# Kernel optimization log

Measured on AMD Instinct MI355X. Metric: run time of the kernel, lower is better.

The kernel has to match this reference:

```python
import jax, jax.numpy as jnp
import numpy as np

EPS = 1e-7
ROUTING_ITERS = 3

def squash(s, axis=-1):
    # v = (|s|^2 / (1+|s|^2)) * s / |s|
    sq = jnp.sum(jnp.square(s), axis=axis, keepdims=True)
    return (sq / (1.0 + sq)) * s / jnp.sqrt(sq + EPS)

def setup_inputs() -> dict:
    key = jax.random.key(0)
    k1, k2 = jax.random.split(key)
    B, NI, DI = 64, 2048, 8      # batch, input capsules, input capsule dim
    NC, DC = 32, 16              # output capsules, output capsule dim
    x = jax.random.normal(k1, (B, NI, DI), dtype=jnp.float32)
    W = jax.random.normal(k2, (NC, NI, DC, DI), dtype=jnp.float32) * 0.05
    return {"x": x, "W": W}

def reference(x, W):
    # x: [B, NI, DI], W: [NC, NI, DC, DI]
    # tf.einsum('iabc,abdc->iabd') == project each input capsule per output capsule
    u = jnp.einsum('bif,cidf->bcid', x, W)          # [B, NC, NI, DC]
    B, NC, NI, DC = u.shape
    b = jnp.zeros((B, NC, NI, 1), dtype=u.dtype)
    v = None
    for _ in range(ROUTING_ITERS):
        c = jax.nn.softmax(b, axis=1)                # coupling over output capsules
        s = jnp.sum(c * u, axis=2, keepdims=True)    # [B, NC, 1, DC]
        v = squash(s, axis=-1)                       # [B, NC, 1, DC]
        # original: reduce_sum(matmul(u, tile(v)^T), axis=3) == NI * <u_i, v>
        agree = jnp.sum(u * v, axis=-1, keepdims=True)  # [B, NC, NI, 1]
        b = b + NI * agree
    return jnp.squeeze(v, axis=2)                    # [B, NC, DC]
```

## Files before the change

### kernel.cpp

```cpp
#include <hip/hip_runtime.h>

#define NI 2048
#define NB 64
#define NC 32
#define DC 16
#define DI 8

static constexpr float SQ_EPS = 1e-7f;

typedef float f8 __attribute__((ext_vector_type(8)));

template <int MODE>
__global__
__attribute__((amdgpu_flat_work_group_size(256, 256), amdgpu_waves_per_eu(2, 2)))
void route_pass(
    const float* __restrict__ x, const float* __restrict__ W,
    const float* __restrict__ veff, float* __restrict__ partial)
{
    __shared__ float4 wbuf[4224];
    __shared__ float4 xbuf[128];

    const int tid   = threadIdx.x;
    const int wave  = tid >> 6;
    const int lane  = tid & 63;
    const int c     = lane & 31;
    const int dg    = lane >> 5;
    const int brel0 = wave * 4;
    const int b0    = blockIdx.y * 16 + brel0;

    f8 s0 = {}, s1 = {}, s2 = {}, s3 = {};

    f8 va = {}, vb = {}, vc = {}, vd = {};
    if (MODE == 1) {
        va = *reinterpret_cast<const f8*>(veff + (((size_t)(b0+0)*2 + dg)*32 + c)*8);
        vb = *reinterpret_cast<const f8*>(veff + (((size_t)(b0+1)*2 + dg)*32 + c)*8);
        vc = *reinterpret_cast<const f8*>(veff + (((size_t)(b0+2)*2 + dg)*32 + c)*8);
        vd = *reinterpret_cast<const f8*>(veff + (((size_t)(b0+3)*2 + dg)*32 + c)*8);
    }

    for (int oct = 0; oct < 4; ++oct) {
        const int i0 = blockIdx.x * 16 + oct * 4;
        __syncthreads();
        {
            const int k  = tid & 31;
            const int p0 = tid >> 5;
            const int k10 = k & 15, kdg = k >> 4;
            for (int r = 0; r < 16; ++r) {
                const int p  = r * 8 + p0;
                const int cc = p >> 2;
                const int il = p & 3;
                wbuf[((il * 16 + k10) * 2 + kdg) * 33 + cc] =
                    reinterpret_cast<const float4*>(W)[
                        ((size_t)cc * NI + i0 + il) * 32 + k];
            }
        }
        if (tid < 128) {
            const int k    = tid & 7;
            const int brel = tid >> 3;
            xbuf[brel * 8 + k] = reinterpret_cast<const float4*>(x)[
                ((size_t)(blockIdx.y * 16 + brel) * NI + i0) * 2 + k];
        }
        __syncthreads();

        for (int il = 0; il < 4; ++il) {
            const float4 xa0 = xbuf[(brel0+0)*8 + il*2], xa1 = xbuf[(brel0+0)*8 + il*2+1];
            const float4 xb0 = xbuf[(brel0+1)*8 + il*2], xb1 = xbuf[(brel0+1)*8 + il*2+1];
            const float4 xc0 = xbuf[(brel0+2)*8 + il*2], xc1 = xbuf[(brel0+2)*8 + il*2+1];
            const float4 xd0 = xbuf[(brel0+3)*8 + il*2], xd1 = xbuf[(brel0+3)*8 + il*2+1];

            f8 u0 = {}, u1 = {}, u2 = {}, u3 = {};
#pragma unroll
            for (int dd = 0; dd < 8; ++dd) {
                const float4 wl = wbuf[((il*16 + dd*2    )*2 + dg)*33 + c];
                const float4 wh = wbuf[((il*16 + dd*2 + 1)*2 + dg)*33 + c];
                u0[dd] = wl.x*xa0.x + wl.y*xa0.y + wl.z*xa0.z + wl.w*xa0.w
                       + wh.x*xa1.x + wh.y*xa1.y + wh.z*xa1.z + wh.w*xa1.w;
                u1[dd] = wl.x*xb0.x + wl.y*xb0.y + wl.z*xb0.z + wl.w*xb0.w
                       + wh.x*xb1.x + wh.y*xb1.y + wh.z*xb1.z + wh.w*xb1.w;
                u2[dd] = wl.x*xc0.x + wl.y*xc0.y + wl.z*xc0.z + wl.w*xc0.w
                       + wh.x*xc1.x + wh.y*xc1.y + wh.z*xc1.z + wh.w*xc1.w;
                u3[dd] = wl.x*xd0.x + wl.y*xd0.y + wl.z*xd0.z + wl.w*xd0.w
                       + wh.x*xd1.x + wh.y*xd1.y + wh.z*xd1.z + wh.w*xd1.w;
            }

            if (MODE == 0) {
                const float cu = 1.0f / 32.0f;
                s0 += u0 * cu; s1 += u1 * cu; s2 += u2 * cu; s3 += u3 * cu;
            } else {
#pragma unroll
                for (int pr = 0; pr < 2; ++pr) {
                    const f8& ue = pr ? u2 : u0;
                    const f8& uo = pr ? u3 : u1;
                    const f8& ve = pr ? vc : va;
                    const f8& vo = pr ? vd : vb;
                    float pe = 0.0f, po = 0.0f;
#pragma unroll
                    for (int k = 0; k < 8; ++k) {
                        pe += ue[k] * ve[k];
                        po += uo[k] * vo[k];
                    }
                    const float send = (dg == 0) ? po : pe;
                    const float recv = __shfl_xor(send, 32);
                    float a = ((dg == 0) ? pe : po) + recv;
                    float m = a;
#pragma unroll
                    for (int off = 16; off >= 1; off >>= 1)
                        m = fmaxf(m, __shfl_xor(m, off));
                    const float e = __expf(a - m);
                    float t = e;
#pragma unroll
                    for (int off = 16; off >= 1; off >>= 1)
                        t += __shfl_xor(t, off);
                    const float mine  = e / t;
                    const float other = __shfl_xor(mine, 32);
                    const float ce = (dg == 0) ? mine : other;
                    const float co = (dg == 0) ? other : mine;
                    if (pr == 0) { s0 += u0 * ce; s1 += u1 * co; }
                    else         { s2 += u2 * ce; s3 += u3 * co; }
                }
            }
        }
    }

    {
        const int pblk = blockIdx.y * gridDim.x + blockIdx.x;
        float* gp = partial +
            (((size_t)pblk * 16 + brel0) * 128 + dg * 64 + c * 2) * 4;
        *reinterpret_cast<f8*>(gp)        = s0;
        *reinterpret_cast<f8*>(gp +  512) = s1;
        *reinterpret_cast<f8*>(gp + 1024) = s2;
        *reinterpret_cast<f8*>(gp + 1536) = s3;
    }
}

__global__ __launch_bounds__(128) void reduce_squash(
    const float* __restrict__ partial, float* __restrict__ veff,
    float* __restrict__ out, int phase)
{
    const int b  = blockIdx.x;
    const int c  = (threadIdx.x >> 2) & 31;
    const int dq = threadIdx.x & 3;

    const float* base = partial
        + ((size_t)(b >> 4) * 2048 + (b & 15)) * 512
        + (dq >> 1) * 256 + c * 8 + (dq & 1) * 4;
    float4 acc = make_float4(0.f, 0.f, 0.f, 0.f);
#pragma unroll 8
    for (int ib = 0; ib < 128; ++ib) {
        const float4 p = *reinterpret_cast<const float4*>(base + (size_t)ib * 8192);
        acc.x += p.x; acc.y += p.y; acc.z += p.z; acc.w += p.w;
    }

    float sq = acc.x*acc.x + acc.y*acc.y + acc.z*acc.z + acc.w*acc.w;
    sq += __shfl_xor(sq, 1);
    sq += __shfl_xor(sq, 2);
    const float scale = sq / ((1.0f + sq) * sqrtf(sq + SQ_EPS));

    if (phase == 3) {
        float4* op = reinterpret_cast<float4*>(out + ((size_t)b * NC + c) * DC + dq * 4);
        *op = make_float4(scale*acc.x, scale*acc.y, scale*acc.z, scale*acc.w);
    } else {
        const float ns = scale * (float)NI;
        float4* vp = reinterpret_cast<float4*>(
            veff + (((size_t)b * 2 + (dq >> 1)) * 32 + c) * 8 + (dq & 1) * 4);
        if (phase == 1) {
            *vp = make_float4(ns*acc.x, ns*acc.y, ns*acc.z, ns*acc.w);
        } else {
            float4 old = *vp;
            *vp = make_float4(old.x + ns*acc.x, old.y + ns*acc.y,
                              old.z + ns*acc.z, old.w + ns*acc.w);
        }
    }
}

extern "C" void kernel_launch(void* const* d_in, const int* in_sizes, int n_in,
                              void* d_out, int out_size, void* d_ws, size_t ws_size,
                              hipStream_t stream) {
    (void)in_sizes; (void)n_in; (void)out_size; (void)ws_size;
    const float* x = (const float*)d_in[0];
    const float* W = (const float*)d_in[1];

    float* partial = (float*)d_ws;
    float* veff    = (float*)d_out;

    const dim3 grid(128, 4);

    route_pass<0><<<grid, 256, 0, stream>>>(x, W, nullptr, partial);
    reduce_squash<<<64, 128, 0, stream>>>(partial, veff, nullptr, 1);

    route_pass<1><<<grid, 256, 0, stream>>>(x, W, veff, partial);
    reduce_squash<<<64, 128, 0, stream>>>(partial, veff, nullptr, 2);

    route_pass<1><<<grid, 256, 0, stream>>>(x, W, veff, partial);
    reduce_squash<<<64, 128, 0, stream>>>(partial, nullptr, (float*)d_out, 3);
}
```

Before: 201.2 us.

## Double-buffer W tiles with register prefetch and widen grid and reduction

The route pass now streams one input capsule at a time through a double-buffered LDS tile. The next capsule's W slice is prefetched into registers while the current one is computed, and all x values for the block are loaded once up front. The grid can grow to 256 input-capsule blocks when the workspace is large enough, occupancy is raised to 3 waves per EU, and the reduce kernel splits its partial-sum reduction across 4 thread groups combined in shared memory. The aim is to hide global load latency and add parallelism. In exchange there are two barriers per capsule, more register pressure, and twice as many partials to reduce.

```diff
diff --git a/kernel.cpp b/kernel.cpp
--- a/kernel.cpp
+++ b/kernel.cpp
@@ -12,24 +12,27 @@
 
 template <int MODE>
 __global__
-__attribute__((amdgpu_flat_work_group_size(256, 256), amdgpu_waves_per_eu(2, 2)))
+__attribute__((amdgpu_flat_work_group_size(256, 256), amdgpu_waves_per_eu(3, 3)))
 void route_pass(
     const float* __restrict__ x, const float* __restrict__ W,
     const float* __restrict__ veff, float* __restrict__ partial)
 {
-    __shared__ float4 wbuf[4224];
-    __shared__ float4 xbuf[128];
-
-    const int tid   = threadIdx.x;
-    const int wave  = tid >> 6;
-    const int lane  = tid & 63;
-    const int c     = lane & 31;
-    const int dg    = lane >> 5;
+    __shared__ float4 wtile[2][1056];
+    __shared__ float4 xbuf[512];
+
+    const int ncap = NI / gridDim.x;
+    const int lgn2 = __builtin_ctz(ncap) + 1;
+    const int tid  = threadIdx.x;
+    const int wave = tid >> 6;
+    const int lane = tid & 63;
+    const int c    = lane & 31;
+    const int dg   = lane >> 5;
     const int brel0 = wave * 4;
-    const int b0    = blockIdx.y * 16 + brel0;
+    const int b0g  = blockIdx.y * 16;
+    const int b0   = b0g + brel0;
+    const int i0   = blockIdx.x * ncap;
 
     f8 s0 = {}, s1 = {}, s2 = {}, s3 = {};
-
     f8 va = {}, vb = {}, vc = {}, vd = {};
     if (MODE == 1) {
         va = *reinterpret_cast<const f8*>(veff + (((size_t)(b0+0)*2 + dg)*32 + c)*8);
@@ -38,41 +41,53 @@
         vd = *reinterpret_cast<const f8*>(veff + (((size_t)(b0+3)*2 + dg)*32 + c)*8);
     }
 
-    for (int oct = 0; oct < 4; ++oct) {
-        const int i0 = blockIdx.x * 16 + oct * 4;
-        __syncthreads();
+    const float4* Wf4 = reinterpret_cast<const float4*>(W);
+    const float4* Xf4 = reinterpret_cast<const float4*>(x);
+    const int kk  = tid & 31;
+    const int cc0 = tid >> 5;
+    const int sb  = ((kk & 15) * 2 + (kk >> 4)) * 33;
+
+    for (int idx = tid; idx < (16 << lgn2); idx += 256) {
+        const int brel = idx >> lgn2;
+        const int rem  = idx & ((1 << lgn2) - 1);
+        xbuf[brel * 32 + rem] =
+            Xf4[((size_t)(b0g + brel) * NI + i0 + (rem >> 1)) * 2 + (rem & 1)];
+    }
+    {
+        float4 t0 = Wf4[((size_t)(cc0     ) * NI + i0) * 32 + kk];
+        float4 t1 = Wf4[((size_t)(cc0 +  8) * NI + i0) * 32 + kk];
+        float4 t2 = Wf4[((size_t)(cc0 + 16) * NI + i0) * 32 + kk];
+        float4 t3 = Wf4[((size_t)(cc0 + 24) * NI + i0) * 32 + kk];
+        wtile[0][sb + cc0     ] = t0;
+        wtile[0][sb + cc0 +  8] = t1;
+        wtile[0][sb + cc0 + 16] = t2;
+        wtile[0][sb + cc0 + 24] = t3;
+    }
+    __syncthreads();
+
+    for (int cap = 0; cap < ncap; ++cap) {
+        float4 t0, t1, t2, t3;
+        const bool more = (cap + 1 < ncap);
+        if (more) {
+            const int ip = i0 + cap + 1;
+            t0 = Wf4[((size_t)(cc0     ) * NI + ip) * 32 + kk];
+            t1 = Wf4[((size_t)(cc0 +  8) * NI + ip) * 32 + kk];
+            t2 = Wf4[((size_t)(cc0 + 16) * NI + ip) * 32 + kk];
+            t3 = Wf4[((size_t)(cc0 + 24) * NI + ip) * 32 + kk];
+        }
+
         {
-            const int k  = tid & 31;
-            const int p0 = tid >> 5;
-            const int k10 = k & 15, kdg = k >> 4;
-            for (int r = 0; r < 16; ++r) {
-                const int p  = r * 8 + p0;
-                const int cc = p >> 2;
-                const int il = p & 3;
-                wbuf[((il * 16 + k10) * 2 + kdg) * 33 + cc] =
-                    reinterpret_cast<const float4*>(W)[
-                        ((size_t)cc * NI + i0 + il) * 32 + k];
-            }
-        }
-        if (tid < 128) {
-            const int k    = tid & 7;
-            const int brel = tid >> 3;
-            xbuf[brel * 8 + k] = reinterpret_cast<const float4*>(x)[
-                ((size_t)(blockIdx.y * 16 + brel) * NI + i0) * 2 + k];
-        }
-        __syncthreads();
-
-        for (int il = 0; il < 4; ++il) {
-            const float4 xa0 = xbuf[(brel0+0)*8 + il*2], xa1 = xbuf[(brel0+0)*8 + il*2+1];
-            const float4 xb0 = xbuf[(brel0+1)*8 + il*2], xb1 = xbuf[(brel0+1)*8 + il*2+1];
-            const float4 xc0 = xbuf[(brel0+2)*8 + il*2], xc1 = xbuf[(brel0+2)*8 + il*2+1];
-            const float4 xd0 = xbuf[(brel0+3)*8 + il*2], xd1 = xbuf[(brel0+3)*8 + il*2+1];
+            const float4* wt = wtile[cap & 1];
+            const float4 xa0 = xbuf[(brel0+0)*32 + cap*2], xa1 = xbuf[(brel0+0)*32 + cap*2 + 1];
+            const float4 xb0 = xbuf[(brel0+1)*32 + cap*2], xb1 = xbuf[(brel0+1)*32 + cap*2 + 1];
+            const float4 xc0 = xbuf[(brel0+2)*32 + cap*2], xc1 = xbuf[(brel0+2)*32 + cap*2 + 1];
+            const float4 xd0 = xbuf[(brel0+3)*32 + cap*2], xd1 = xbuf[(brel0+3)*32 + cap*2 + 1];
 
             f8 u0 = {}, u1 = {}, u2 = {}, u3 = {};
 #pragma unroll
             for (int dd = 0; dd < 8; ++dd) {
-                const float4 wl = wbuf[((il*16 + dd*2    )*2 + dg)*33 + c];
-                const float4 wh = wbuf[((il*16 + dd*2 + 1)*2 + dg)*33 + c];
+                const float4 wl = wt[(4*dd     + dg)*33 + c];
+                const float4 wh = wt[(4*dd + 2 + dg)*33 + c];
                 u0[dd] = wl.x*xa0.x + wl.y*xa0.y + wl.z*xa0.z + wl.w*xa0.w
                        + wh.x*xa1.x + wh.y*xa1.y + wh.z*xa1.z + wh.w*xa1.w;
                 u1[dd] = wl.x*xb0.x + wl.y*xb0.y + wl.z*xb0.z + wl.w*xb0.w
@@ -120,6 +135,16 @@
                 }
             }
         }
+
+        if (more) {
+            __syncthreads();
+            float4* wn = wtile[(cap + 1) & 1];
+            wn[sb + cc0     ] = t0;
+            wn[sb + cc0 +  8] = t1;
+            wn[sb + cc0 + 16] = t2;
+            wn[sb + cc0 + 24] = t3;
+            __syncthreads();
+        }
     }
 
     {
@@ -133,42 +158,57 @@
     }
 }
 
-__global__ __launch_bounds__(128) void reduce_squash(
+__global__ __launch_bounds__(512) void reduce_squash(
     const float* __restrict__ partial, float* __restrict__ veff,
-    float* __restrict__ out, int phase)
+    float* __restrict__ out, int phase, int nib)
 {
-    const int b  = blockIdx.x;
-    const int c  = (threadIdx.x >> 2) & 31;
-    const int dq = threadIdx.x & 3;
+    __shared__ float4 red[512];
+    const int b     = blockIdx.x;
+    const int tid   = threadIdx.x;
+    const int part  = tid >> 7;
+    const int inner = tid & 127;
+    const int c     = inner >> 2;
+    const int dq    = inner & 3;
+    const int chunk = nib >> 2;
 
     const float* base = partial
-        + ((size_t)(b >> 4) * 2048 + (b & 15)) * 512
-        + (dq >> 1) * 256 + c * 8 + (dq & 1) * 4;
+        + ((size_t)(b >> 4) * nib + part * chunk) * 8192
+        + (b & 15) * 512 + (dq >> 1) * 256 + c * 8 + (dq & 1) * 4;
     float4 acc = make_float4(0.f, 0.f, 0.f, 0.f);
 #pragma unroll 8
-    for (int ib = 0; ib < 128; ++ib) {
+    for (int ib = 0; ib < chunk; ++ib) {
         const float4 p = *reinterpret_cast<const float4*>(base + (size_t)ib * 8192);
         acc.x += p.x; acc.y += p.y; acc.z += p.z; acc.w += p.w;
     }
-
-    float sq = acc.x*acc.x + acc.y*acc.y + acc.z*acc.z + acc.w*acc.w;
-    sq += __shfl_xor(sq, 1);
-    sq += __shfl_xor(sq, 2);
-    const float scale = sq / ((1.0f + sq) * sqrtf(sq + SQ_EPS));
-
-    if (phase == 3) {
-        float4* op = reinterpret_cast<float4*>(out + ((size_t)b * NC + c) * DC + dq * 4);
-        *op = make_float4(scale*acc.x, scale*acc.y, scale*acc.z, scale*acc.w);
-    } else {
-        const float ns = scale * (float)NI;
-        float4* vp = reinterpret_cast<float4*>(
-            veff + (((size_t)b * 2 + (dq >> 1)) * 32 + c) * 8 + (dq & 1) * 4);
-        if (phase == 1) {
-            *vp = make_float4(ns*acc.x, ns*acc.y, ns*acc.z, ns*acc.w);
+    red[tid] = acc;
+    __syncthreads();
+    if (part == 0) {
+        const float4 r1 = red[inner + 128], r2 = red[inner + 256], r3 = red[inner + 384];
+        acc.x += r1.x + r2.x + r3.x;
+        acc.y += r1.y + r2.y + r3.y;
+        acc.z += r1.z + r2.z + r3.z;
+        acc.w += r1.w + r2.w + r3.w;
+
+        float sq = acc.x*acc.x + acc.y*acc.y + acc.z*acc.z + acc.w*acc.w;
+        sq += __shfl_xor(sq, 1);
+        sq += __shfl_xor(sq, 2);
+        const float scale = sq / ((1.0f + sq) * sqrtf(sq + SQ_EPS));
+
+        if (phase == 3) {
+            float4* op = reinterpret_cast<float4*>(
+                out + ((size_t)b * NC + c) * DC + dq * 4);
+            *op = make_float4(scale*acc.x, scale*acc.y, scale*acc.z, scale*acc.w);
         } else {
-            float4 old = *vp;
-            *vp = make_float4(old.x + ns*acc.x, old.y + ns*acc.y,
-                              old.z + ns*acc.z, old.w + ns*acc.w);
+            const float ns = scale * (float)NI;
+            float4* vp = reinterpret_cast<float4*>(
+                veff + (((size_t)b * 2 + (dq >> 1)) * 32 + c) * 8 + (dq & 1) * 4);
+            if (phase == 1) {
+                *vp = make_float4(ns*acc.x, ns*acc.y, ns*acc.z, ns*acc.w);
+            } else {
+                float4 old = *vp;
+                *vp = make_float4(old.x + ns*acc.x, old.y + ns*acc.y,
+                                  old.z + ns*acc.z, old.w + ns*acc.w);
+            }
         }
     }
 }
@@ -176,21 +216,22 @@
 extern "C" void kernel_launch(void* const* d_in, const int* in_sizes, int n_in,
                               void* d_out, int out_size, void* d_ws, size_t ws_size,
                               hipStream_t stream) {
-    (void)in_sizes; (void)n_in; (void)out_size; (void)ws_size;
+    (void)in_sizes; (void)n_in; (void)out_size;
     const float* x = (const float*)d_in[0];
     const float* W = (const float*)d_in[1];
 
     float* partial = (float*)d_ws;
     float* veff    = (float*)d_out;
 
-    const dim3 grid(128, 4);
+    const int nib = (ws_size >= (size_t)4 * 256 * 8192 * 4) ? 256 : 128;
+    const dim3 grid(nib, 4);
 
     route_pass<0><<<grid, 256, 0, stream>>>(x, W, nullptr, partial);
-    reduce_squash<<<64, 128, 0, stream>>>(partial, veff, nullptr, 1);
+    reduce_squash<<<64, 512, 0, stream>>>(partial, veff, nullptr, 1, nib);
 
     route_pass<1><<<grid, 256, 0, stream>>>(x, W, veff, partial);
-    reduce_squash<<<64, 128, 0, stream>>>(partial, veff, nullptr, 2);
+    reduce_squash<<<64, 512, 0, stream>>>(partial, veff, nullptr, 2, nib);
 
     route_pass<1><<<grid, 256, 0, stream>>>(x, W, veff, partial);
-    reduce_squash<<<64, 128, 0, stream>>>(partial, nullptr, (float*)d_out, 3);
+    reduce_squash<<<64, 512, 0, stream>>>(partial, nullptr, (float*)d_out, 3, nib);
 }
```

Measured after the change: 262.3 us. 30.4% more time.
